# Kernel optimization log

Measured on AMD Instinct MI355X. Metric: run time of the kernel, lower is better.

The kernel has to match this reference:

```python
import jax, jax.numpy as jnp
import numpy as np

B, L, D_IN, H, C = 64, 2048, 400, 200, 32
NEG = 1e12


def setup_inputs() -> dict:
    key = jax.random.key(0)
    k1, k2, k3, k4, k5 = jax.random.split(key, 5)
    x = jax.random.normal(k1, (B, L, D_IN), dtype=jnp.float32)
    category_bias = jax.random.normal(k2, (B, L, C), dtype=jnp.float32)
    att_mask = (jax.random.uniform(k3, (B, L)) > 0.2).astype(jnp.float32)
    # glorot-uniform-ish scales
    W_proj = jax.random.normal(k4, (D_IN, H), dtype=jnp.float32) * np.float32(np.sqrt(2.0 / (D_IN + H)))
    context = jax.random.normal(k5, (C, H), dtype=jnp.float32) * np.float32(np.sqrt(2.0 / (C + H)))
    lamada = jnp.zeros((1,), dtype=jnp.float32)
    return {"x": x, "category_bias": category_bias, "att_mask": att_mask,
            "W_proj": W_proj, "context": context, "lamada": lamada}


def reference(x, category_bias, att_mask, W_proj, context, lamada):
    # proj: [B, L, H] = tanh(x @ W_proj)  (Dense, no bias)
    proj = jnp.tanh(jnp.einsum("bld,dh->blh", x, W_proj))
    # scores vs learned context vectors: [B, L, C]
    weights = jnp.einsum("blh,ch->blc", proj, context) + lamada * category_bias
    # [B, C, L]
    weights = jnp.transpose(weights, (0, 2, 1))
    # additive large-negative mask, then softmax over sequence
    weights = weights - (1.0 - att_mask[:, None, :]) * NEG
    weights = jax.nn.softmax(weights, axis=-1)
    # poly representation: [B, C, D_IN]
    return jnp.einsum("bcl,bld->bcd", weights, x)
```

## Files before the change

kernel.cpp:

```cpp
#include <hip/hip_runtime.h>
#include <cmath>
#include <cstdint>

#define B_ 64
#define L_ 2048
#define DIN 400
#define H_ 200
#define C_ 32
#define NEGBIG 1e12f
#define KC1 13
#define NT1 13
#define KC2 7
#define MT2 2
#define NLC 16
#define NS 32

typedef _Float16 half8 __attribute__((ext_vector_type(8)));
typedef float f32x4 __attribute__((ext_vector_type(4)));
typedef unsigned int uint4v __attribute__((ext_vector_type(4)));

__device__ __align__(16) _Float16 g_wfrag[KC1 * NT1 * 512];
__device__ __align__(16) _Float16 g_cfrag[KC2 * MT2 * 512];

static __device__ __forceinline__ f32x4 mfma16(half8 a, half8 b, f32x4 c) {
  return __builtin_amdgcn_mfma_f32_16x16x32_f16(a, b, c, 0, 0, 0);
}

static __device__ __forceinline__ float fast_tanh(float v) {
  const float e = __expf(2.0f * v);
  return 1.0f - 2.0f / (e + 1.0f);
}

__global__ __launch_bounds__(64) void k_prep(const float* __restrict__ Wp,
                                             const float* __restrict__ ctx)
{
  const int lane = threadIdx.x;
  const int bid = blockIdx.x;
  if (bid < KC1 * NT1) {
    const int q = bid / NT1, nt = bid % NT1;
    const int kb = q * 32 + (lane >> 4) * 8;
    const int n  = nt * 16 + (lane & 15);
    half8 h;
#pragma unroll
    for (int j = 0; j < 8; ++j) {
      const int k = kb + j;
      const float v = (k < DIN && n < H_) ? Wp[(size_t)k * H_ + n] : 0.0f;
      h[j] = (_Float16)v;
    }
    *reinterpret_cast<half8*>(&g_wfrag[((size_t)bid << 9) + (lane << 3)]) = h;
  } else {
    const int r = bid - KC1 * NT1;
    const int c  = (r % MT2) * 16 + (lane & 15);
    const int hb = (r / MT2) * 32 + (lane >> 4) * 8;
    half8 h;
#pragma unroll
    for (int j = 0; j < 8; ++j) {
      const int hh = hb + j;
      const float v = (hh < H_) ? ctx[(size_t)c * H_ + hh] : 0.0f;
      h[j] = (_Float16)v;
    }
    *reinterpret_cast<half8*>(&g_cfrag[((size_t)r << 9) + (lane << 3)]) = h;
  }
}

__global__ __launch_bounds__(256, 4) void k_fused(
    const float* __restrict__ x,
    const float* __restrict__ cb,
    const float* __restrict__ mask,
    const float* __restrict__ lam,
    _Float16* __restrict__ O,
    float* __restrict__ stats)
{
  __shared__ __align__(16) unsigned char shm[38144];
  half8* smemv = reinterpret_cast<half8*>(shm);
  unsigned int* xsw = reinterpret_cast<unsigned int*>(shm);
  _Float16* Pl = reinterpret_cast<_Float16*>(shm + 32768);
  float* redw  = reinterpret_cast<float*>(shm + 36864);
  float* mfin  = reinterpret_cast<float*>(shm + 37376);
  float* denf  = reinterpret_cast<float*>(shm + 37504);

  const int tid  = threadIdx.x;
  const int lane = tid & 63;
  const int w    = __builtin_amdgcn_readfirstlane(tid >> 6);
  const int b    = blockIdx.y;
  const int split = blockIdx.x;
  const int l0   = split * 64;
  const int oct  = lane >> 4;

  f32x4 acc[NT1];
#pragma unroll
  for (int nt = 0; nt < NT1; ++nt) acc[nt] = f32x4{0.f, 0.f, 0.f, 0.f};

  const float* xrow =
      x + ((size_t)b * L_ + l0 + w * 16 + (lane & 15)) * DIN + oct * 8;

  for (int i = w; i < NT1; i += 4) {
    const _Float16* gp = g_wfrag + (((size_t)i) << 9) + (lane << 3);
    __builtin_amdgcn_global_load_lds(
        (const __attribute__((address_space(1))) void*)gp,
        (__attribute__((address_space(3))) void*)(smemv + i * 64),
        16, 0, 0);
  }
  __builtin_amdgcn_sched_barrier(0);
  float4 cur0 = *reinterpret_cast<const float4*>(xrow);
  float4 cur1 = *reinterpret_cast<const float4*>(xrow + 4);

#pragma unroll
  for (int q = 0; q < KC1; ++q) {
    asm volatile("s_waitcnt vmcnt(2)\n\ts_barrier" ::: "memory");

    float4 nx0 = float4{0.f, 0.f, 0.f, 0.f};
    float4 nx1 = float4{0.f, 0.f, 0.f, 0.f};
    if (q < KC1 - 1) {
      const int nb = ((q + 1) & 1) * 832;
      for (int i = w; i < NT1; i += 4) {
        const _Float16* gp =
            g_wfrag + (((size_t)((q + 1) * NT1 + i)) << 9) + (lane << 3);
        __builtin_amdgcn_global_load_lds(
            (const __attribute__((address_space(1))) void*)gp,
            (__attribute__((address_space(3))) void*)(smemv + nb + i * 64),
            16, 0, 0);
      }
      __builtin_amdgcn_sched_barrier(0);
      const int k0 = (q + 1) * 32 + oct * 8;
      if (k0 + 7 < DIN) {
        nx0 = *reinterpret_cast<const float4*>(xrow + (q + 1) * 32);
        nx1 = *reinterpret_cast<const float4*>(xrow + (q + 1) * 32 + 4);
      }
    }

    float fa[8] = {cur0.x, cur0.y, cur0.z, cur0.w,
                   cur1.x, cur1.y, cur1.z, cur1.w};
    half8 ah;
#pragma unroll
    for (int j = 0; j < 8; ++j) ah[j] = (_Float16)fa[j];

    const int base = (q & 1) * 832;
    __builtin_amdgcn_s_setprio(1);
#pragma unroll
    for (int nt = 0; nt < NT1; ++nt) {
      const half8 bh = smemv[base + nt * 64 + lane];
      acc[nt] = mfma16(ah, bh, acc[nt]);
    }
    __builtin_amdgcn_s_setprio(0);
    cur0 = nx0;
    cur1 = nx1;
  }

  __syncthreads();
  if (lane >= 32) {
    half8 z = {};
    smemv[(24 + w) * 64 + lane] = z;
  }
  _Float16* Pp = reinterpret_cast<_Float16*>(shm);
#pragma unroll
  for (int nt = 0; nt < NT1; ++nt) {
    const int h   = nt * 16 + (lane & 15);
    const int q2  = h >> 5;
    const int lpw = ((h >> 3) & 3) << 4;
    const int jj  = h & 7;
#pragma unroll
    for (int reg = 0; reg < 4; ++reg) {
      const int t = ((lane >> 4) << 2) + reg;
      const float p = fast_tanh(acc[nt][reg]);
      Pp[(size_t)(((q2 * 4 + w) * 64) + lpw + t) * 8 + jj] = (_Float16)p;
    }
  }

  f32x4 s0 = f32x4{0.f, 0.f, 0.f, 0.f};
  f32x4 s1 = f32x4{0.f, 0.f, 0.f, 0.f};
  __builtin_amdgcn_s_setprio(1);
#pragma unroll
  for (int q2 = 0; q2 < KC2; ++q2) {
    const half8 pb = smemv[(q2 * 4 + w) * 64 + lane];
    const half8 c0 = *reinterpret_cast<const half8*>(
        g_cfrag + (((size_t)(q2 * 2)) << 9) + (lane << 3));
    const half8 c1 = *reinterpret_cast<const half8*>(
        g_cfrag + (((size_t)(q2 * 2 + 1)) << 9) + (lane << 3));
    s0 = mfma16(c0, pb, s0);
    s1 = mfma16(c1, pb, s1);
  }
  __builtin_amdgcn_s_setprio(0);

  const int tok = (w << 4) | (lane & 15);
  const size_t bl = (size_t)b * L_ + l0 + tok;
  const float lamv = lam[0];
  const float mk = (1.0f - mask[bl]) * NEGBIG;
  const int cq = oct << 2;
  const float4 cb0 = *reinterpret_cast<const float4*>(cb + bl * C_ + cq);
  const float4 cb1 = *reinterpret_cast<const float4*>(cb + bl * C_ + 16 + cq);
  float sv[8];
  sv[0] = s0[0] + lamv * cb0.x - mk;  sv[1] = s0[1] + lamv * cb0.y - mk;
  sv[2] = s0[2] + lamv * cb0.z - mk;  sv[3] = s0[3] + lamv * cb0.w - mk;
  sv[4] = s1[0] + lamv * cb1.x - mk;  sv[5] = s1[1] + lamv * cb1.y - mk;
  sv[6] = s1[2] + lamv * cb1.z - mk;  sv[7] = s1[3] + lamv * cb1.w - mk;
  int cidx[8];
#pragma unroll
  for (int r = 0; r < 8; ++r) cidx[r] = (r < 4) ? (cq + r) : (16 + cq + r - 4);

  float mx[8];
#pragma unroll
  for (int r = 0; r < 8; ++r) {
    float v = sv[r];
#pragma unroll
    for (int off = 1; off < 16; off <<= 1) v = fmaxf(v, __shfl_xor(v, off));
    mx[r] = v;
  }
  if ((lane & 15) == 0) {
#pragma unroll
    for (int r = 0; r < 8; ++r) redw[w * 32 + cidx[r]] = mx[r];
  }
  __syncthreads();
  if (tid < 32)
    mfin[tid] = fmaxf(fmaxf(redw[tid], redw[32 + tid]),
                      fmaxf(redw[64 + tid], redw[96 + tid]));
  __syncthreads();

  float pd[8];
#pragma unroll
  for (int r = 0; r < 8; ++r) {
    const float p = __expf(sv[r] - mfin[cidx[r]]);
    pd[r] = p;
    const int c = cidx[r];
    Pl[c * 64 + ((((tok >> 3) ^ (c & 7)) & 7) << 3) + (tok & 7)] = (_Float16)p;
  }
#pragma unroll
  for (int r = 0; r < 8; ++r) {
    float v = pd[r];
#pragma unroll
    for (int off = 1; off < 16; off <<= 1) v += __shfl_xor(v, off);
    pd[r] = v;
  }
  if ((lane & 15) == 0) {
#pragma unroll
    for (int r = 0; r < 8; ++r) redw[w * 32 + cidx[r]] = pd[r];
  }
  __syncthreads();
  if (tid < 32)
    denf[tid] = redw[tid] + redw[32 + tid] + redw[64 + tid] + redw[96 + tid];

  const int ntile0w = (w == 0) ? 0 : (1 + 6 * w);
  const int NTWv   = w ? 6 : 7;
  const int n   = lane & 15;

  f32x4 oacc[2][7];
#pragma unroll
  for (int ct = 0; ct < 2; ++ct)
#pragma unroll
    for (int nt = 0; nt < 7; ++nt) oacc[ct][nt] = f32x4{0.f, 0.f, 0.f, 0.f};

  const float* xb = x + ((size_t)b * L_ + l0) * DIN;

  for (int h = 0; h < 2; ++h) {
    __syncthreads();
    for (int s = 0; s < 7; ++s) {
      const int i = s * 256 + tid;
      if (i < 1600) {
        const int lp = i / 100, qd = i - lp * 100;
        const float* src = xb + (size_t)(h * 32 + 2 * lp) * DIN + 4 * qd;
        const float4 r0 = *reinterpret_cast<const float4*>(src);
        const float4 r1 = *reinterpret_cast<const float4*>(src + DIN);
#pragma unroll
        for (int k = 0; k < 4; ++k) {
          const int d = 4 * qd + k;
          const int sw = ((d >> 2) ^ (d >> 4)) & 3;
          const int col = (((lp >> 2) ^ sw) << 2) | (lp & 3);
          const _Float16 h0 = (_Float16)r0[k];
          const _Float16 h1 = (_Float16)r1[k];
          unsigned int pk = (unsigned int)__builtin_bit_cast(unsigned short, h0) |
                            ((unsigned int)__builtin_bit_cast(unsigned short, h1) << 16);
          xsw[d * 20 + col] = pk;
        }
      }
    }
    __syncthreads();

    half8 aP[2];
#pragma unroll
    for (int ct = 0; ct < 2; ++ct) {
      const int c = ct * 16 + n;
      aP[ct] = *reinterpret_cast<const half8*>(
          &Pl[c * 64 + (((((h << 2) | oct) ^ (c & 7)) & 7) << 3)]);
    }
    __builtin_amdgcn_s_setprio(1);
#pragma unroll
    for (int nt = 0; nt < 7; ++nt) {
      if (nt < NTWv) {
        const int d0 = (ntile0w + nt) * 16 + n;
        const int sw = ((d0 >> 2) ^ (d0 >> 4)) & 3;
        const half8 bh = *reinterpret_cast<const half8*>(
            &xsw[d0 * 20 + ((oct ^ sw) << 2)]);
        oacc[0][nt] = mfma16(aP[0], bh, oacc[0][nt]);
        oacc[1][nt] = mfma16(aP[1], bh, oacc[1][nt]);
      }
    }
    __builtin_amdgcn_s_setprio(0);
  }

  _Float16* Ob = O + ((size_t)(b * NS + split) * C_) * DIN;
#pragma unroll
  for (int nt = 0; nt < 7; ++nt) {
    if (nt < NTWv) {
      const int d = (ntile0w + nt) * 16 + n;
#pragma unroll
      for (int ct = 0; ct < 2; ++ct) {
#pragma unroll
        for (int reg = 0; reg < 4; ++reg) {
          const int c = ct * 16 + oct * 4 + reg;
          Ob[(size_t)c * DIN + d] = (_Float16)oacc[ct][nt][reg];
        }
      }
    }
  }
  if (tid < 32) {
    float* st = stats + (size_t)(b * NS + split) * 64;
    st[tid]      = mfin[tid];
    st[32 + tid] = denf[tid];
  }
}

__global__ __launch_bounds__(256) void k_combine(
    const _Float16* __restrict__ O, const float* __restrict__ stats,
    float* __restrict__ out)
{
  const int idx = blockIdx.x * 256 + threadIdx.x;
  const int b  = idx / (C_ * 50);
  const int rm = idx - b * (C_ * 50);
  const int c  = rm / 50;
  const int dq = rm - c * 50;

  const float* st = stats + (size_t)b * NS * 64;
  float M = -3.4e38f;
#pragma unroll
  for (int s = 0; s < NS; ++s) M = fmaxf(M, st[s * 64 + c]);
  float wsc[NS];
  float denom = 0.f;
#pragma unroll
  for (int s = 0; s < NS; ++s) {
    const float e = __expf(st[s * 64 + c] - M);
    wsc[s] = e;
    denom += e * st[s * 64 + 32 + c];
  }
  const float inv = 1.0f / denom;

  float o[8] = {};
  const uint4v* Op = reinterpret_cast<const uint4v*>(
      O + ((size_t)(b * NS) * C_ + c) * DIN + dq * 8);
#pragma unroll
  for (int s = 0; s < NS; ++s) {
    const uint4v v = Op[(size_t)s * (C_ * DIN / 8)];
#pragma unroll
    for (int j = 0; j < 4; ++j) {
      o[2 * j]     += wsc[s] * (float)__builtin_bit_cast(_Float16, (unsigned short)(v[j] & 0xffff));
      o[2 * j + 1] += wsc[s] * (float)__builtin_bit_cast(_Float16, (unsigned short)(v[j] >> 16));
    }
  }
  float* op = out + ((size_t)(b * C_) + c) * DIN + dq * 8;
  *reinterpret_cast<float4*>(op)     = float4{o[0]*inv, o[1]*inv, o[2]*inv, o[3]*inv};
  *reinterpret_cast<float4*>(op + 4) = float4{o[4]*inv, o[5]*inv, o[6]*inv, o[7]*inv};
}

__global__ __launch_bounds__(256, 5) void k_scores(
    const float* __restrict__ x, const float* __restrict__ cb,
    const float* __restrict__ mask, const float* __restrict__ lam,
    float* __restrict__ S)
{
  __shared__ half8 smemv[1792];
  const int tid  = threadIdx.x;
  const int lane = tid & 63;
  const int w    = __builtin_amdgcn_readfirstlane(tid >> 6);
  const int b    = blockIdx.y;
  const int l0   = blockIdx.x * 64;
  const int oct  = lane >> 4;

  f32x4 acc[NT1];
#pragma unroll
  for (int nt = 0; nt < NT1; ++nt) acc[nt] = f32x4{0.f, 0.f, 0.f, 0.f};
  const float* xrow =
      x + ((size_t)b * L_ + l0 + w * 16 + (lane & 15)) * DIN + oct * 8;
  for (int i = w; i < NT1; i += 4) {
    const _Float16* gp = g_wfrag + (((size_t)i) << 9) + (lane << 3);
    __builtin_amdgcn_global_load_lds(
        (const __attribute__((address_space(1))) void*)gp,
        (__attribute__((address_space(3))) void*)(smemv + i * 64), 16, 0, 0);
  }
  __builtin_amdgcn_sched_barrier(0);
  float4 cur0 = *reinterpret_cast<const float4*>(xrow);
  float4 cur1 = *reinterpret_cast<const float4*>(xrow + 4);
#pragma unroll
  for (int q = 0; q < KC1; ++q) {
    asm volatile("s_waitcnt vmcnt(2)\n\ts_barrier" ::: "memory");
    float4 nx0 = float4{0.f, 0.f, 0.f, 0.f};
    float4 nx1 = float4{0.f, 0.f, 0.f, 0.f};
    if (q < KC1 - 1) {
      const int nb = ((q + 1) & 1) * 832;
      for (int i = w; i < NT1; i += 4) {
        const _Float16* gp =
            g_wfrag + (((size_t)((q + 1) * NT1 + i)) << 9) + (lane << 3);
        __builtin_amdgcn_global_load_lds(
            (const __attribute__((address_space(1))) void*)gp,
            (__attribute__((address_space(3))) void*)(smemv + nb + i * 64),
            16, 0, 0);
      }
      __builtin_amdgcn_sched_barrier(0);
      const int k0 = (q + 1) * 32 + oct * 8;
      if (k0 + 7 < DIN) {
        nx0 = *reinterpret_cast<const float4*>(xrow + (q + 1) * 32);
        nx1 = *reinterpret_cast<const float4*>(xrow + (q + 1) * 32 + 4);
      }
    }
    float fa[8] = {cur0.x, cur0.y, cur0.z, cur0.w,
                   cur1.x, cur1.y, cur1.z, cur1.w};
    half8 ah;
#pragma unroll
    for (int j = 0; j < 8; ++j) ah[j] = (_Float16)fa[j];
    const int base = (q & 1) * 832;
#pragma unroll
    for (int nt = 0; nt < NT1; ++nt) {
      const half8 bh = smemv[base + nt * 64 + lane];
      acc[nt] = mfma16(ah, bh, acc[nt]);
    }
    cur0 = nx0; cur1 = nx1;
  }
  __syncthreads();
  if (lane >= 32) { half8 z = {}; smemv[(24 + w) * 64 + lane] = z; }
  _Float16* Pp = reinterpret_cast<_Float16*>(smemv);
#pragma unroll
  for (int nt = 0; nt < NT1; ++nt) {
    const int h = nt * 16 + (lane & 15);
    const int q2 = h >> 5, lpw = ((h >> 3) & 3) << 4, jj = h & 7;
#pragma unroll
    for (int reg = 0; reg < 4; ++reg) {
      const int t = ((lane >> 4) << 2) + reg;
      Pp[(size_t)(((q2 * 4 + w) * 64) + lpw + t) * 8 + jj] =
          (_Float16)fast_tanh(acc[nt][reg]);
    }
  }
  f32x4 s0 = f32x4{0.f, 0.f, 0.f, 0.f};
  f32x4 s1 = f32x4{0.f, 0.f, 0.f, 0.f};
#pragma unroll
  for (int q2 = 0; q2 < KC2; ++q2) {
    const half8 pb = smemv[(q2 * 4 + w) * 64 + lane];
    const half8 c0 = *reinterpret_cast<const half8*>(
        g_cfrag + (((size_t)(q2 * 2)) << 9) + (lane << 3));
    const half8 c1 = *reinterpret_cast<const half8*>(
        g_cfrag + (((size_t)(q2 * 2 + 1)) << 9) + (lane << 3));
    s0 = mfma16(c0, pb, s0);
    s1 = mfma16(c1, pb, s1);
  }
  const int tok = (w << 4) | (lane & 15);
  const size_t bl = (size_t)b * L_ + l0 + tok;
  const float lamv = lam[0];
  const float mk = (1.0f - mask[bl]) * NEGBIG;
  const int cq = (lane >> 4) << 2;
  const float4 cb0 = *reinterpret_cast<const float4*>(cb + bl * C_ + cq);
  const float4 cb1 = *reinterpret_cast<const float4*>(cb + bl * C_ + 16 + cq);
  float* Sp = S + (size_t)b * C_ * L_ + l0 + tok;
  Sp[(size_t)(cq + 0) * L_] = s0[0] + lamv * cb0.x - mk;
  Sp[(size_t)(cq + 1) * L_] = s0[1] + lamv * cb0.y - mk;
  Sp[(size_t)(cq + 2) * L_] = s0[2] + lamv * cb0.z - mk;
  Sp[(size_t)(cq + 3) * L_] = s0[3] + lamv * cb0.w - mk;
  Sp[(size_t)(16 + cq + 0) * L_] = s1[0] + lamv * cb1.x - mk;
  Sp[(size_t)(16 + cq + 1) * L_] = s1[1] + lamv * cb1.y - mk;
  Sp[(size_t)(16 + cq + 2) * L_] = s1[2] + lamv * cb1.z - mk;
  Sp[(size_t)(16 + cq + 3) * L_] = s1[3] + lamv * cb1.w - mk;
}

__global__ __launch_bounds__(256) void k_softmax(float* __restrict__ S,
                                                 _Float16* __restrict__ wh)
{
  const int row = blockIdx.x;
  float* R = S + (size_t)row * L_;
  const int t8 = threadIdx.x * 8;
  const float4 va = *reinterpret_cast<const float4*>(R + t8);
  const float4 vb = *reinterpret_cast<const float4*>(R + t8 + 4);
  float v[8] = {va.x, va.y, va.z, va.w, vb.x, vb.y, vb.z, vb.w};
  float m = -3.4e38f;
#pragma unroll
  for (int j = 0; j < 8; ++j) m = fmaxf(m, v[j]);
#pragma unroll
  for (int o = 32; o > 0; o >>= 1) m = fmaxf(m, __shfl_xor(m, o));
  __shared__ float red[4];
  const int wid = threadIdx.x >> 6;
  if ((threadIdx.x & 63) == 0) red[wid] = m;
  __syncthreads();
  m = fmaxf(fmaxf(red[0], red[1]), fmaxf(red[2], red[3]));
  __syncthreads();
  float s = 0.f;
#pragma unroll
  for (int j = 0; j < 8; ++j) { v[j] = __expf(v[j] - m); s += v[j]; }
#pragma unroll
  for (int o = 32; o > 0; o >>= 1) s += __shfl_xor(s, o);
  if ((threadIdx.x & 63) == 0) red[wid] = s;
  __syncthreads();
  s = red[0] + red[1] + red[2] + red[3];
  const float inv = 1.0f / s;
  if (wh != nullptr) {
    uint4v pk;
#pragma unroll
    for (int p = 0; p < 4; ++p) {
      const _Float16 h0 = (_Float16)(v[2 * p] * inv);
      const _Float16 h1 = (_Float16)(v[2 * p + 1] * inv);
      pk[p] = (unsigned int)__builtin_bit_cast(unsigned short, h0) |
              ((unsigned int)__builtin_bit_cast(unsigned short, h1) << 16);
    }
    *reinterpret_cast<uint4v*>(wh + (size_t)row * L_ + t8) = pk;
  } else {
#pragma unroll
    for (int j = 0; j < 8; ++j) R[t8 + j] = v[j] * inv;
  }
}

__global__ __launch_bounds__(512, 4) void k_out_mfma(
    const float* __restrict__ x, const _Float16* __restrict__ wh,
    _Float16* __restrict__ part)
{
  __shared__ unsigned int xsw[400 * 20];
  __shared__ unsigned int ws16[32][16];
  const int tid  = threadIdx.x;
  const int lane = tid & 63;
  const int w    = __builtin_amdgcn_readfirstlane(tid >> 6);
  const int b    = blockIdx.y;
  const int kq   = blockIdx.x;
  const int l0b  = kq * (L_ / NLC);
  const int ntile0 = (w < 7) ? w * 3 : 21;
  const int NTW    = (w < 7) ? 3 : 4;
  const int n   = lane & 15;
  const int oct = lane >> 4;
  f32x4 acc[4][2];
#pragma unroll
  for (int i = 0; i < 4; ++i) {
    acc[i][0] = f32x4{0.f, 0.f, 0.f, 0.f};
    acc[i][1] = f32x4{0.f, 0.f, 0.f, 0.f};
  }
  const float* xb = x + ((size_t)b * L_ + l0b) * DIN;
  const unsigned int* whb = reinterpret_cast<const unsigned int*>(
      wh + (size_t)b * C_ * L_ + l0b);
  float4 r0[4], r1[4];
  unsigned int wreg;
#pragma unroll
  for (int s = 0; s < 4; ++s) {
    const int i = s * 512 + tid;
    if (s < 3 || i < 1600) {
      const int lp = i / 100, qd = i - lp * 100;
      const float* src = xb + (size_t)(2 * lp) * DIN + 4 * qd;
      r0[s] = *reinterpret_cast<const float4*>(src);
      r1[s] = *reinterpret_cast<const float4*>(src + DIN);
    }
  }
  wreg = whb[((size_t)(tid >> 4) * L_) / 2 + (tid & 15)];
  const int NCH = (L_ / NLC) / 32;
  for (int ch = 0; ch < NCH; ++ch) {
    __syncthreads();
#pragma unroll
    for (int s = 0; s < 4; ++s) {
      const int i = s * 512 + tid;
      if (s < 3 || i < 1600) {
        const int lp = i / 100, qd = i - lp * 100;
#pragma unroll
        for (int k = 0; k < 4; ++k) {
          const int d = 4 * qd + k;
          const int sw = ((d >> 2) ^ (d >> 4)) & 3;
          const int col = (((lp >> 2) ^ sw) << 2) | (lp & 3);
          const _Float16 h0 = (_Float16)r0[s][k];
          const _Float16 h1 = (_Float16)r1[s][k];
          unsigned int pk = (unsigned int)__builtin_bit_cast(unsigned short, h0) |
                            ((unsigned int)__builtin_bit_cast(unsigned short, h1) << 16);
          xsw[d * 20 + col] = pk;
        }
      }
    }
    ws16[tid >> 4][tid & 15] = wreg;
    __syncthreads();
    if (ch + 1 < NCH) {
      const float* xc = xb + (size_t)((ch + 1) * 32) * DIN;
#pragma unroll
      for (int s = 0; s < 4; ++s) {
        const int i = s * 512 + tid;
        if (s < 3 || i < 1600) {
          const int lp = i / 100, qd = i - lp * 100;
          const float* src = xc + (size_t)(2 * lp) * DIN + 4 * qd;
          r0[s] = *reinterpret_cast<const float4*>(src);
          r1[s] = *reinterpret_cast<const float4*>(src + DIN);
        }
      }
      wreg = whb[((size_t)(tid >> 4) * L_ + (ch + 1) * 32) / 2 + (tid & 15)];
    }
    union { uint4v u; half8 h; } a0c, a1c;
    a0c.u = *reinterpret_cast<const uint4v*>(&ws16[n][oct * 4]);
    a1c.u = *reinterpret_cast<const uint4v*>(&ws16[n + 16][oct * 4]);
    const half8 a0 = a0c.h;
    const half8 a1 = a1c.h;
#pragma unroll
    for (int nt = 0; nt < 4; ++nt) {
      if (nt < NTW) {
        const int d0 = (ntile0 + nt) * 16 + n;
        const int sw = ((d0 >> 2) ^ (d0 >> 4)) & 3;
        const half8 bh = *reinterpret_cast<const half8*>(
            &xsw[d0 * 20 + ((oct ^ sw) << 2)]);
        acc[nt][0] = mfma16(a0, bh, acc[nt][0]);
        acc[nt][1] = mfma16(a1, bh, acc[nt][1]);
      }
    }
  }
  _Float16* pb = part + ((size_t)(b * NLC + kq) * C_) * DIN;
#pragma unroll
  for (int nt = 0; nt < 4; ++nt) {
    if (nt < NTW) {
      const int d = (ntile0 + nt) * 16 + n;
#pragma unroll
      for (int mt = 0; mt < 2; ++mt) {
#pragma unroll
        for (int reg = 0; reg < 4; ++reg) {
          const int c = mt * 16 + oct * 4 + reg;
          pb[(size_t)c * DIN + d] = (_Float16)acc[nt][mt][reg];
        }
      }
    }
  }
}

__global__ __launch_bounds__(256) void k_out_reduce(
    const _Float16* __restrict__ part, float* __restrict__ out)
{
  const int idx = blockIdx.x * 256 + threadIdx.x;
  const int per_b = C_ * DIN / 8;
  const int b = idx / per_b;
  const int r = idx - b * per_b;
  const uint4v* p = reinterpret_cast<const uint4v*>(part) +
                    (size_t)b * NLC * per_b + r;
  float s[8] = {};
#pragma unroll
  for (int lc = 0; lc < NLC; ++lc) {
    const uint4v v = p[(size_t)lc * per_b];
#pragma unroll
    for (int j = 0; j < 4; ++j) {
      s[2 * j]     += (float)__builtin_bit_cast(_Float16, (unsigned short)(v[j] & 0xffff));
      s[2 * j + 1] += (float)__builtin_bit_cast(_Float16, (unsigned short)(v[j] >> 16));
    }
  }
  float* o = out + (size_t)idx * 8;
  *reinterpret_cast<float4*>(o)     = float4{s[0], s[1], s[2], s[3]};
  *reinterpret_cast<float4*>(o + 4) = float4{s[4], s[5], s[6], s[7]};
}

extern "C" void kernel_launch(void* const* d_in, const int* in_sizes, int n_in,
                              void* d_out, int out_size, void* d_ws, size_t ws_size,
                              hipStream_t stream)
{
  const float* x    = (const float*)d_in[0];
  const float* cb   = (const float*)d_in[1];
  const float* mask = (const float*)d_in[2];
  const float* Wp   = (const float*)d_in[3];
  const float* ctx  = (const float*)d_in[4];
  const float* lam  = (const float*)d_in[5];
  float* out = (float*)d_out;

  k_prep<<<dim3(KC1 * NT1 + KC2 * MT2), 64, 0, stream>>>(Wp, ctx);

  const size_t O_bytes = (size_t)B_ * NS * C_ * DIN * sizeof(_Float16);
  const size_t st_bytes = (size_t)B_ * NS * 64 * sizeof(float);
  if (ws_size >= O_bytes + st_bytes) {
    _Float16* O = (_Float16*)d_ws;
    float* stats = (float*)((char*)d_ws + O_bytes);
    k_fused<<<dim3(NS, B_), 256, 0, stream>>>(x, cb, mask, lam, O, stats);
    k_combine<<<dim3(B_ * C_ * 50 / 256), 256, 0, stream>>>(O, stats, out);
    return;
  }

  const size_t part_bytes = (size_t)B_ * NLC * C_ * DIN * sizeof(_Float16);
  float* S = (float*)d_ws;
  _Float16* part = (_Float16*)d_ws;
  _Float16* wh = (_Float16*)((char*)d_ws + part_bytes);
  k_scores<<<dim3(L_ / 64, B_), 256, 0, stream>>>(x, cb, mask, lam, S);
  k_softmax<<<dim3(B_ * C_), 256, 0, stream>>>(S, wh);
  k_out_mfma<<<dim3(NLC, B_), 512, 0, stream>>>(x, wh, part);
  k_out_reduce<<<dim3(B_ * C_ * DIN / 8 / 256), 256, 0, stream>>>(part, out);
}
```

Baseline: 102.3 us.

## Process 128 tokens per block to halve split count and partial outputs

Each block now covers 128 sequence positions, computing the projection and scores in two 64-token sub-passes and running softmax stats and the weighted-sum accumulation over all 128. This halves the number of splits, and with it the partial output tiles and stats that must be written and merged later, and the repeated per-block setup. In exchange the grid has half as many blocks, each doing twice the serial work, and LDS use grows slightly. That could reduce occupancy and parallelism on a large GPU.

```diff
diff --git a/kernel.cpp b/kernel.cpp
--- a/kernel.cpp
+++ b/kernel.cpp
@@ -13,7 +13,7 @@
 #define KC2 7
 #define MT2 2
 #define NLC 16
-#define NS 32
+#define NS 16
 
 typedef _Float16 half8 __attribute__((ext_vector_type(8)));
 typedef float f32x4 __attribute__((ext_vector_type(4)));
@@ -71,137 +71,146 @@
     _Float16* __restrict__ O,
     float* __restrict__ stats)
 {
-  __shared__ __align__(16) unsigned char shm[38144];
+  __shared__ __align__(16) unsigned char shm[40960];
   half8* smemv = reinterpret_cast<half8*>(shm);
   unsigned int* xsw = reinterpret_cast<unsigned int*>(shm);
-  _Float16* Pl = reinterpret_cast<_Float16*>(shm + 32768);
-  float* redw  = reinterpret_cast<float*>(shm + 36864);
-  float* mfin  = reinterpret_cast<float*>(shm + 37376);
-  float* denf  = reinterpret_cast<float*>(shm + 37504);
+  _Float16* Pl = reinterpret_cast<_Float16*>(shm + 32000);
+  float* redw  = reinterpret_cast<float*>(shm + 40192);
+  float* mfin  = reinterpret_cast<float*>(shm + 40704);
+  float* denf  = reinterpret_cast<float*>(shm + 40832);
 
   const int tid  = threadIdx.x;
   const int lane = tid & 63;
   const int w    = __builtin_amdgcn_readfirstlane(tid >> 6);
   const int b    = blockIdx.y;
   const int split = blockIdx.x;
-  const int l0   = split * 64;
+  const int l0   = split * 128;
   const int oct  = lane >> 4;
-
-  f32x4 acc[NT1];
-#pragma unroll
-  for (int nt = 0; nt < NT1; ++nt) acc[nt] = f32x4{0.f, 0.f, 0.f, 0.f};
-
-  const float* xrow =
-      x + ((size_t)b * L_ + l0 + w * 16 + (lane & 15)) * DIN + oct * 8;
-
-  for (int i = w; i < NT1; i += 4) {
-    const _Float16* gp = g_wfrag + (((size_t)i) << 9) + (lane << 3);
-    __builtin_amdgcn_global_load_lds(
-        (const __attribute__((address_space(1))) void*)gp,
-        (__attribute__((address_space(3))) void*)(smemv + i * 64),
-        16, 0, 0);
-  }
-  __builtin_amdgcn_sched_barrier(0);
-  float4 cur0 = *reinterpret_cast<const float4*>(xrow);
-  float4 cur1 = *reinterpret_cast<const float4*>(xrow + 4);
-
-#pragma unroll
-  for (int q = 0; q < KC1; ++q) {
-    asm volatile("s_waitcnt vmcnt(2)\n\ts_barrier" ::: "memory");
-
-    float4 nx0 = float4{0.f, 0.f, 0.f, 0.f};
-    float4 nx1 = float4{0.f, 0.f, 0.f, 0.f};
-    if (q < KC1 - 1) {
-      const int nb = ((q + 1) & 1) * 832;
-      for (int i = w; i < NT1; i += 4) {
-        const _Float16* gp =
-            g_wfrag + (((size_t)((q + 1) * NT1 + i)) << 9) + (lane << 3);
-        __builtin_amdgcn_global_load_lds(
-            (const __attribute__((address_space(1))) void*)gp,
-            (__attribute__((address_space(3))) void*)(smemv + nb + i * 64),
-            16, 0, 0);
-      }
-      __builtin_amdgcn_sched_barrier(0);
-      const int k0 = (q + 1) * 32 + oct * 8;
-      if (k0 + 7 < DIN) {
-        nx0 = *reinterpret_cast<const float4*>(xrow + (q + 1) * 32);
-        nx1 = *reinterpret_cast<const float4*>(xrow + (q + 1) * 32 + 4);
-      }
-    }
-
-    float fa[8] = {cur0.x, cur0.y, cur0.z, cur0.w,
-                   cur1.x, cur1.y, cur1.z, cur1.w};
-    half8 ah;
-#pragma unroll
-    for (int j = 0; j < 8; ++j) ah[j] = (_Float16)fa[j];
-
-    const int base = (q & 1) * 832;
+  const int tok  = (w << 4) | (lane & 15);
+  const int cq   = oct << 2;
+  int cidx[8];
+#pragma unroll
+  for (int r = 0; r < 8; ++r) cidx[r] = (r < 4) ? (cq + r) : (16 + cq + r - 4);
+  const float lamv = lam[0];
+
+  float sv2[2][8];
+
+  for (int sub = 0; sub < 2; ++sub) {
+    if (sub) __syncthreads();
+
+    f32x4 acc[NT1];
+#pragma unroll
+    for (int nt = 0; nt < NT1; ++nt) acc[nt] = f32x4{0.f, 0.f, 0.f, 0.f};
+
+    const float* xrow =
+        x + ((size_t)b * L_ + l0 + sub * 64 + w * 16 + (lane & 15)) * DIN + oct * 8;
+
+    for (int i = w; i < NT1; i += 4) {
+      const _Float16* gp = g_wfrag + (((size_t)i) << 9) + (lane << 3);
+      __builtin_amdgcn_global_load_lds(
+          (const __attribute__((address_space(1))) void*)gp,
+          (__attribute__((address_space(3))) void*)(smemv + i * 64),
+          16, 0, 0);
+    }
+    __builtin_amdgcn_sched_barrier(0);
+    float4 cur0 = *reinterpret_cast<const float4*>(xrow);
+    float4 cur1 = *reinterpret_cast<const float4*>(xrow + 4);
+
+#pragma unroll
+    for (int q = 0; q < KC1; ++q) {
+      asm volatile("s_waitcnt vmcnt(2)\n\ts_barrier" ::: "memory");
+
+      float4 nx0 = float4{0.f, 0.f, 0.f, 0.f};
+      float4 nx1 = float4{0.f, 0.f, 0.f, 0.f};
+      if (q < KC1 - 1) {
+        const int nb = ((q + 1) & 1) * 832;
+        for (int i = w; i < NT1; i += 4) {
+          const _Float16* gp =
+              g_wfrag + (((size_t)((q + 1) * NT1 + i)) << 9) + (lane << 3);
+          __builtin_amdgcn_global_load_lds(
+              (const __attribute__((address_space(1))) void*)gp,
+              (__attribute__((address_space(3))) void*)(smemv + nb + i * 64),
+              16, 0, 0);
+        }
+        __builtin_amdgcn_sched_barrier(0);
+        const int k0 = (q + 1) * 32 + oct * 8;
+        if (k0 + 7 < DIN) {
+          nx0 = *reinterpret_cast<const float4*>(xrow + (q + 1) * 32);
+          nx1 = *reinterpret_cast<const float4*>(xrow + (q + 1) * 32 + 4);
+        }
+      }
+
+      float fa[8] = {cur0.x, cur0.y, cur0.z, cur0.w,
+                     cur1.x, cur1.y, cur1.z, cur1.w};
+      half8 ah;
+#pragma unroll
+      for (int j = 0; j < 8; ++j) ah[j] = (_Float16)fa[j];
+
+      const int base = (q & 1) * 832;
+      __builtin_amdgcn_s_setprio(1);
+#pragma unroll
+      for (int nt = 0; nt < NT1; ++nt) {
+        const half8 bh = smemv[base + nt * 64 + lane];
+        acc[nt] = mfma16(ah, bh, acc[nt]);
+      }
+      __builtin_amdgcn_s_setprio(0);
+      cur0 = nx0;
+      cur1 = nx1;
+    }
+
+    __syncthreads();
+    if (lane >= 32) {
+      half8 z = {};
+      smemv[(24 + w) * 64 + lane] = z;
+    }
+    _Float16* Pp = reinterpret_cast<_Float16*>(shm);
+#pragma unroll
+    for (int nt = 0; nt < NT1; ++nt) {
+      const int h   = nt * 16 + (lane & 15);
+      const int q2  = h >> 5;
+      const int lpw = ((h >> 3) & 3) << 4;
+      const int jj  = h & 7;
+#pragma unroll
+      for (int reg = 0; reg < 4; ++reg) {
+        const int t = oct * 4 + reg;
+        const float p = fast_tanh(acc[nt][reg]);
+        Pp[(size_t)(((q2 * 4 + w) * 64) + lpw + t) * 8 + jj] = (_Float16)p;
+      }
+    }
+
+    f32x4 s0 = f32x4{0.f, 0.f, 0.f, 0.f};
+    f32x4 s1 = f32x4{0.f, 0.f, 0.f, 0.f};
     __builtin_amdgcn_s_setprio(1);
 #pragma unroll
-    for (int nt = 0; nt < NT1; ++nt) {
-      const half8 bh = smemv[base + nt * 64 + lane];
-      acc[nt] = mfma16(ah, bh, acc[nt]);
+    for (int q2 = 0; q2 < KC2; ++q2) {
+      const half8 pb = smemv[(q2 * 4 + w) * 64 + lane];
+      const half8 c0 = *reinterpret_cast<const half8*>(
+          g_cfrag + (((size_t)(q2 * 2)) << 9) + (lane << 3));
+      const half8 c1 = *reinterpret_cast<const half8*>(
+          g_cfrag + (((size_t)(q2 * 2 + 1)) << 9) + (lane << 3));
+      s0 = mfma16(c0, pb, s0);
+      s1 = mfma16(c1, pb, s1);
     }
     __builtin_amdgcn_s_setprio(0);
-    cur0 = nx0;
-    cur1 = nx1;
-  }
-
-  __syncthreads();
-  if (lane >= 32) {
-    half8 z = {};
-    smemv[(24 + w) * 64 + lane] = z;
-  }
-  _Float16* Pp = reinterpret_cast<_Float16*>(shm);
-#pragma unroll
-  for (int nt = 0; nt < NT1; ++nt) {
-    const int h   = nt * 16 + (lane & 15);
-    const int q2  = h >> 5;
-    const int lpw = ((h >> 3) & 3) << 4;
-    const int jj  = h & 7;
-#pragma unroll
-    for (int reg = 0; reg < 4; ++reg) {
-      const int t = ((lane >> 4) << 2) + reg;
-      const float p = fast_tanh(acc[nt][reg]);
-      Pp[(size_t)(((q2 * 4 + w) * 64) + lpw + t) * 8 + jj] = (_Float16)p;
-    }
-  }
-
-  f32x4 s0 = f32x4{0.f, 0.f, 0.f, 0.f};
-  f32x4 s1 = f32x4{0.f, 0.f, 0.f, 0.f};
-  __builtin_amdgcn_s_setprio(1);
-#pragma unroll
-  for (int q2 = 0; q2 < KC2; ++q2) {
-    const half8 pb = smemv[(q2 * 4 + w) * 64 + lane];
-    const half8 c0 = *reinterpret_cast<const half8*>(
-        g_cfrag + (((size_t)(q2 * 2)) << 9) + (lane << 3));
-    const half8 c1 = *reinterpret_cast<const half8*>(
-        g_cfrag + (((size_t)(q2 * 2 + 1)) << 9) + (lane << 3));
-    s0 = mfma16(c0, pb, s0);
-    s1 = mfma16(c1, pb, s1);
-  }
-  __builtin_amdgcn_s_setprio(0);
-
-  const int tok = (w << 4) | (lane & 15);
-  const size_t bl = (size_t)b * L_ + l0 + tok;
-  const float lamv = lam[0];
-  const float mk = (1.0f - mask[bl]) * NEGBIG;
-  const int cq = oct << 2;
-  const float4 cb0 = *reinterpret_cast<const float4*>(cb + bl * C_ + cq);
-  const float4 cb1 = *reinterpret_cast<const float4*>(cb + bl * C_ + 16 + cq);
-  float sv[8];
-  sv[0] = s0[0] + lamv * cb0.x - mk;  sv[1] = s0[1] + lamv * cb0.y - mk;
-  sv[2] = s0[2] + lamv * cb0.z - mk;  sv[3] = s0[3] + lamv * cb0.w - mk;
-  sv[4] = s1[0] + lamv * cb1.x - mk;  sv[5] = s1[1] + lamv * cb1.y - mk;
-  sv[6] = s1[2] + lamv * cb1.z - mk;  sv[7] = s1[3] + lamv * cb1.w - mk;
-  int cidx[8];
-#pragma unroll
-  for (int r = 0; r < 8; ++r) cidx[r] = (r < 4) ? (cq + r) : (16 + cq + r - 4);
+
+    const size_t bl = (size_t)b * L_ + l0 + sub * 64 + tok;
+    const float mk = (1.0f - mask[bl]) * NEGBIG;
+    const float4 cb0 = *reinterpret_cast<const float4*>(cb + bl * C_ + cq);
+    const float4 cb1 = *reinterpret_cast<const float4*>(cb + bl * C_ + 16 + cq);
+    sv2[sub][0] = s0[0] + lamv * cb0.x - mk;
+    sv2[sub][1] = s0[1] + lamv * cb0.y - mk;
+    sv2[sub][2] = s0[2] + lamv * cb0.z - mk;
+    sv2[sub][3] = s0[3] + lamv * cb0.w - mk;
+    sv2[sub][4] = s1[0] + lamv * cb1.x - mk;
+    sv2[sub][5] = s1[1] + lamv * cb1.y - mk;
+    sv2[sub][6] = s1[2] + lamv * cb1.z - mk;
+    sv2[sub][7] = s1[3] + lamv * cb1.w - mk;
+  }
 
   float mx[8];
 #pragma unroll
   for (int r = 0; r < 8; ++r) {
-    float v = sv[r];
+    float v = fmaxf(sv2[0][r], sv2[1][r]);
 #pragma unroll
     for (int off = 1; off < 16; off <<= 1) v = fmaxf(v, __shfl_xor(v, off));
     mx[r] = v;
@@ -219,10 +228,13 @@
   float pd[8];
 #pragma unroll
   for (int r = 0; r < 8; ++r) {
-    const float p = __expf(sv[r] - mfin[cidx[r]]);
-    pd[r] = p;
     const int c = cidx[r];
-    Pl[c * 64 + ((((tok >> 3) ^ (c & 7)) & 7) << 3) + (tok & 7)] = (_Float16)p;
+    const int slot = c * 128 + ((((tok >> 3) ^ (c & 7)) & 7) << 3) + (tok & 7);
+    const float p0 = __expf(sv2[0][r] - mfin[c]);
+    const float p1 = __expf(sv2[1][r] - mfin[c]);
+    Pl[slot]      = (_Float16)p0;
+    Pl[slot + 64] = (_Float16)p1;
+    pd[r] = p0 + p1;
   }
 #pragma unroll
   for (int r = 0; r < 8; ++r) {
@@ -251,7 +263,7 @@
 
   const float* xb = x + ((size_t)b * L_ + l0) * DIN;
 
-  for (int h = 0; h < 2; ++h) {
+  for (int h = 0; h < 4; ++h) {
     __syncthreads();
     for (int s = 0; s < 7; ++s) {
       const int i = s * 256 + tid;
@@ -275,12 +287,14 @@
     }
     __syncthreads();
 
+    const int sub = h >> 1;
+    const int kblk = ((h & 1) << 2) | oct;
     half8 aP[2];
 #pragma unroll
     for (int ct = 0; ct < 2; ++ct) {
       const int c = ct * 16 + n;
       aP[ct] = *reinterpret_cast<const half8*>(
-          &Pl[c * 64 + (((((h << 2) | oct) ^ (c & 7)) & 7) << 3)]);
+          &Pl[c * 128 + sub * 64 + (((kblk ^ (c & 7)) & 7) << 3)]);
     }
     __builtin_amdgcn_s_setprio(1);
 #pragma unroll
```

Measured after the change: 197.3 us. 1.93x slower.
